# Kernel optimization log

Measured on AMD Instinct MI355X. Metric: run time of the kernel, lower is better.

The kernel has to match this reference:

```python
import jax, jax.numpy as jnp
import numpy as np

D_MODEL = 1024
N_HEADS = 16
D_K = D_MODEL // N_HEADS
B, S = 2, 2048


def setup_inputs() -> dict:
    key = jax.random.key(0)
    ks = jax.random.split(key, 5)
    sc = 1.0 / np.sqrt(D_MODEL)
    return {
        "x": jax.random.normal(ks[0], (B, S, D_MODEL), dtype=jnp.float32),
        "W_qkv": jax.random.normal(ks[1], (D_MODEL, 3 * D_MODEL), dtype=jnp.float32) * sc,
        "b_qkv": jnp.zeros((3 * D_MODEL,), dtype=jnp.float32),
        "W_out": jax.random.normal(ks[2], (D_MODEL, D_MODEL), dtype=jnp.float32) * sc,
        "b_out": jnp.zeros((D_MODEL,), dtype=jnp.float32),
    }


def reference(x, W_qkv, b_qkv, W_out, b_out):
    Bb, Ss, _ = x.shape
    qkv = x @ W_qkv + b_qkv                     # [B,S,3*D]
    qkv = qkv.reshape(Bb, Ss, 3, N_HEADS, D_K)
    qkv = jnp.transpose(qkv, (2, 0, 3, 1, 4))   # [3,B,H,S,Dk]
    q, k, v = qkv[0], qkv[1], qkv[2]
    scale = jnp.asarray(np.sqrt(D_K), dtype=x.dtype)
    attn = jnp.einsum('bhsd,bhtd->bhst', q, k) / scale  # [B,H,S,S]
    attn = jax.nn.softmax(attn, axis=-1)
    out = jnp.einsum('bhst,bhtd->bhsd', attn, v)        # [B,H,S,Dk]
    out = jnp.transpose(out, (0, 2, 1, 3)).reshape(Bb, Ss, D_MODEL)
    return out @ W_out + b_out
```

## Files before the change

### kernel.cpp

```cpp
#include <hip/hip_runtime.h>

typedef __bf16 bf16x8 __attribute__((ext_vector_type(8)));
typedef __bf16 bf16x4 __attribute__((ext_vector_type(4)));
typedef float f32x4 __attribute__((ext_vector_type(4)));
typedef unsigned short u16;
typedef unsigned short u16x4 __attribute__((ext_vector_type(4)));
typedef unsigned int u32;

__device__ __forceinline__ u16 f2bu(float f) {
  __bf16 h = (__bf16)f;
  return __builtin_bit_cast(u16, h);
}

__device__ __forceinline__ void gld16(const u16* g, const __bf16* lds) {
  __builtin_amdgcn_global_load_lds(
      (const __attribute__((address_space(1))) u32*)(uintptr_t)g,
      (__attribute__((address_space(3))) u32*)(u32)(uintptr_t)lds, 16, 0, 0);
}

__device__ __forceinline__ void tr_tile(const float* __restrict__ in, u16* __restrict__ out,
                                        int R, int C, int bx, int by, int tid) {
  __shared__ u16 t[64][65];
  int tx = tid & 63, ty = tid >> 6;
  int r0 = by * 64, c0 = bx * 64;
  for (int i = 0; i < 16; ++i)
    t[ty + i * 4][tx] = f2bu(in[(size_t)(r0 + ty + i * 4) * C + c0 + tx]);
  __syncthreads();
  for (int i = 0; i < 16; ++i)
    out[(size_t)(c0 + ty + i * 4) * R + r0 + tx] = t[tx][ty + i * 4];
}

__global__ __launch_bounds__(256) void prep(const float* __restrict__ Wqkv,
                                            u16* __restrict__ Wqkv_t,
                                            const float* __restrict__ Wout,
                                            u16* __restrict__ Wout_t,
                                            const float* __restrict__ x,
                                            u16* __restrict__ xb) {
  int id = blockIdx.x, tid = threadIdx.x;
  if (id < 768) {
    tr_tile(Wqkv, Wqkv_t, 1024, 3072, id % 48, id / 48, tid);
  } else if (id < 1024) {
    int id2 = id - 768;
    tr_tile(Wout, Wout_t, 1024, 1024, id2 % 16, id2 / 16, tid);
  } else {
    size_t i = ((size_t)(id - 1024) * 256 + tid) * 8;
    f32x4 a0 = *(const f32x4*)(x + i);
    f32x4 a1 = *(const f32x4*)(x + i + 4);
    bf16x8 v;
    for (int j = 0; j < 4; ++j) { v[j] = (__bf16)a0[j]; v[j + 4] = (__bf16)a1[j]; }
    *(bf16x8*)(xb + i) = v;
  }
}

template <int MODE, int TM, int TN, int MT, int NT, int XM, int XN>
__global__ __launch_bounds__(256) void gemm_bt(const u16* __restrict__ A,
                                               const u16* __restrict__ Bt,
                                               const float* __restrict__ bias,
                                               void* __restrict__ O0v,
                                               u16* __restrict__ O1,
                                               u16* __restrict__ O2,
                                               int M, int N, int K) {
  constexpr int NI = TM / 32;
  constexpr int NJ = TN / 32;
  constexpr int AE = TM * 32;
  constexpr int BE = TN * 32;
  __shared__ __bf16 smem[2 * (AE + BE)];

  int tid = threadIdx.x;
  int w = tid >> 6, lane = tid & 63, quad = lane >> 4, l16 = lane & 15;
  int wr = w >> 1, wc = w & 1;

  int id = blockIdx.x;
  int xcd = id & 7, s0i = id >> 3;
  int mg = xcd % (MT / XM), ng = xcd / (MT / XM);
  int sm = s0i % XM, sn = s0i / XM;
  int m0 = (mg * XM + sm) * TM, n0 = (ng * XN + sn) * TN;

  int srow = w * 16 + (lane >> 2);
  int sch = (lane & 3) ^ ((lane >> 3) & 3);
  const u16* Ag = A + (size_t)(m0 + srow) * K + sch * 8;
  const u16* Bg = Bt + (size_t)(n0 + srow) * K + sch * 8;

  int swl = (quad ^ ((l16 >> 1) & 3)) << 3;

  f32x4 acc[NI][NJ] = {};

#define GLD_STEP(c, kk)                                                          \
  {                                                                              \
    for (int p = 0; p < TM / 64; ++p)                                            \
      gld16(Ag + (size_t)p * 64 * K + (kk), smem + (c) * (AE + BE) + w * 512 + p * 2048); \
    for (int p = 0; p < TN / 64; ++p)                                            \
      gld16(Bg + (size_t)p * 64 * K + (kk), smem + (c) * (AE + BE) + AE + w * 512 + p * 2048); \
  }

  GLD_STEP(0, 0);
  int NS = K / 32;
  for (int s = 0; s < NS; ++s) {
    int cur = s & 1;
    __syncthreads();
    if (s + 1 < NS) GLD_STEP(1 - cur, (s + 1) * 32);
    const __bf16* Asub = smem + cur * (AE + BE);
    const __bf16* Bsub = Asub + AE;
    bf16x8 af[NI], bfr[NJ];
    for (int i = 0; i < NI; ++i)
      af[i] = *(const bf16x8*)(Asub + (wr * (TM / 2) + i * 16 + l16) * 32 + swl);
    for (int j = 0; j < NJ; ++j)
      bfr[j] = *(const bf16x8*)(Bsub + (wc * (TN / 2) + j * 16 + l16) * 32 + swl);
    for (int i = 0; i < NI; ++i)
      for (int j = 0; j < NJ; ++j)
        acc[i][j] = __builtin_amdgcn_mfma_f32_16x16x32_bf16(af[i], bfr[j], acc[i][j], 0, 0, 0);
  }
#undef GLD_STEP

  if (MODE == 0) {
    float* O0 = (float*)O0v;
    for (int j = 0; j < NJ; ++j) {
      int n = n0 + wc * (TN / 2) + j * 16 + l16;
      float bv = bias[n];
      for (int i = 0; i < NI; ++i) {
        int mb = m0 + wr * (TM / 2) + i * 16 + quad * 4;
        for (int r = 0; r < 4; ++r)
          O0[(size_t)(mb + r) * N + n] = acc[i][j][r] + bv;
      }
    }
  } else {
    u16* O0 = (u16*)O0v;
    constexpr float QSC = 0.125f * 1.44269504f;
    for (int j = 0; j < NJ; ++j) {
      int n = n0 + wc * (TN / 2) + j * 16 + l16;
      int which = n >> 10, rem = n & 1023, h = rem >> 6, d = rem & 63;
      float bv = bias[n];
      for (int i = 0; i < NI; ++i) {
        int m = m0 + wr * (TM / 2) + i * 16 + quad * 4;
        int b = m >> 11, s = m & 2047;
        if (which == 2) {
          u16x4 val;
          for (int r = 0; r < 4; ++r) val[r] = f2bu(acc[i][j][r] + bv);
          *(u16x4*)(O2 + (((size_t)(b * 16 + h)) * 64 + d) * 2048 + s) = val;
        } else {
          u16* Od = which ? O1 : O0;
          float sc = which ? 1.f : QSC;
          for (int r = 0; r < 4; ++r)
            Od[(((size_t)(b * 16 + h)) * 2048 + (s + r)) * 64 + d] = f2bu((acc[i][j][r] + bv) * sc);
        }
      }
    }
  }
}

__global__ __launch_bounds__(256, 2) void flash_attn(const u16* __restrict__ Q,
                                                     const u16* __restrict__ K,
                                                     const u16* __restrict__ Vt,
                                                     u16* __restrict__ AO) {
  constexpr int S = 2048;
  __shared__ __bf16 Ks[2][64 * 64];
  __shared__ __bf16 Vs[2][64 * 64];
  __shared__ __bf16 Ps[4][32 * 64];

  int bh = blockIdx.x, qbase = blockIdx.y * 128;
  int tid = threadIdx.x, w = tid >> 6, lane = tid & 63, quad = lane >> 4, l16 = lane & 15;

  const u16* Qh = Q + (size_t)bh * S * 64;
  const u16* Kh = K + (size_t)bh * S * 64;
  const u16* Vh = Vt + (size_t)bh * 64 * S;

  int qrowA = qbase + w * 32 + l16;
  int qrowB = qrowA + 16;
  bf16x8 qf0a = *(const bf16x8*)(Qh + (size_t)qrowA * 64 + quad * 8);
  bf16x8 qf1a = *(const bf16x8*)(Qh + (size_t)qrowA * 64 + 32 + quad * 8);
  bf16x8 qf0b = *(const bf16x8*)(Qh + (size_t)qrowB * 64 + quad * 8);
  bf16x8 qf1b = *(const bf16x8*)(Qh + (size_t)qrowB * 64 + 32 + quad * 8);

  bf16x8 vone;
#pragma unroll
  for (int j = 0; j < 8; ++j) vone[j] = (__bf16)1.0f;

  int r0s = tid >> 3, b0s = tid & 7;
  int r1s = r0s + 32;
  int ko0 = r0s * 64 + ((b0s ^ (r0s & 7)) << 3);
  int ko1 = r1s * 64 + ((b0s ^ (r1s & 7)) << 3);

  bf16x8 kr0, kr1, vr0, vr1;
#define LOAD_TILE(tb)                                                   \
  {                                                                     \
    kr0 = *(const bf16x8*)(Kh + (size_t)((tb) + r0s) * 64 + b0s * 8);   \
    kr1 = *(const bf16x8*)(Kh + (size_t)((tb) + r1s) * 64 + b0s * 8);   \
    vr0 = *(const bf16x8*)(Vh + (size_t)r0s * S + (tb) + b0s * 8);      \
    vr1 = *(const bf16x8*)(Vh + (size_t)r1s * S + (tb) + b0s * 8);      \
  }
#define STORE_TILE(c)                                                   \
  {                                                                     \
    *(bf16x8*)(&Ks[c][ko0]) = kr0;                                      \
    *(bf16x8*)(&Ks[c][ko1]) = kr1;                                      \
    *(bf16x8*)(&Vs[c][ko0]) = vr0;                                      \
    *(bf16x8*)(&Vs[c][ko1]) = vr1;                                      \
  }

  LOAD_TILE(0);
  STORE_TILE(0);
  LOAD_TILE(64);
  __syncthreads();

  f32x4 oA[4] = {};
  f32x4 oB[4] = {};
  f32x4 lfA = {};
  f32x4 lfB = {};
  int xr = l16 & 7;
  int pw_baseA = l16 * 64 + (quad & 1) * 4;
  int pw_baseB = (l16 + 16) * 64 + (quad & 1) * 4;
  int pw_blk = quad >> 1;

  for (int it = 0; it < S / 64; ++it) {
    int c = it & 1;
    if (it + 1 < S / 64) STORE_TILE(1 - c);
    if (it + 2 < S / 64) LOAD_TILE((it + 2) * 64);

    for (int nt = 0; nt < 4; ++nt) {
      const __bf16* kb = &Ks[c][(nt * 16 + l16) * 64];
      bf16x8 kf0 = *(const bf16x8*)(kb + ((quad ^ xr) << 3));
      bf16x8 kf1 = *(const bf16x8*)(kb + (((quad + 4) ^ xr) << 3));
      f32x4 ca = {0.f, 0.f, 0.f, 0.f};
      f32x4 cb = {0.f, 0.f, 0.f, 0.f};
      ca = __builtin_amdgcn_mfma_f32_16x16x32_bf16(kf0, qf0a, ca, 0, 0, 0);
      cb = __builtin_amdgcn_mfma_f32_16x16x32_bf16(kf0, qf0b, cb, 0, 0, 0);
      ca = __builtin_amdgcn_mfma_f32_16x16x32_bf16(kf1, qf1a, ca, 0, 0, 0);
      cb = __builtin_amdgcn_mfma_f32_16x16x32_bf16(kf1, qf1b, cb, 0, 0, 0);
      bf16x4 pka, pkb;
#pragma unroll
      for (int r = 0; r < 4; ++r) {
        pka[r] = (__bf16)__builtin_amdgcn_exp2f(ca[r]);
        pkb[r] = (__bf16)__builtin_amdgcn_exp2f(cb[r]);
      }
      int pc = (((nt * 2 + pw_blk) ^ xr) << 3);
      *(bf16x4*)(&Ps[w][pw_baseA + pc]) = pka;
      *(bf16x4*)(&Ps[w][pw_baseB + pc]) = pkb;
    }

    bf16x8 pf0a = *(const bf16x8*)(&Ps[w][l16 * 64 + ((quad ^ xr) << 3)]);
    bf16x8 pf1a = *(const bf16x8*)(&Ps[w][l16 * 64 + (((quad + 4) ^ xr) << 3)]);
    bf16x8 pf0b = *(const bf16x8*)(&Ps[w][(l16 + 16) * 64 + ((quad ^ xr) << 3)]);
    bf16x8 pf1b = *(const bf16x8*)(&Ps[w][(l16 + 16) * 64 + (((quad + 4) ^ xr) << 3)]);

    lfA = __builtin_amdgcn_mfma_f32_16x16x32_bf16(pf0a, vone, lfA, 0, 0, 0);
    lfA = __builtin_amdgcn_mfma_f32_16x16x32_bf16(pf1a, vone, lfA, 0, 0, 0);
    lfB = __builtin_amdgcn_mfma_f32_16x16x32_bf16(pf0b, vone, lfB, 0, 0, 0);
    lfB = __builtin_amdgcn_mfma_f32_16x16x32_bf16(pf1b, vone, lfB, 0, 0, 0);

    for (int dt = 0; dt < 4; ++dt) {
      const __bf16* vb = &Vs[c][(dt * 16 + l16) * 64];
      bf16x8 v0 = *(const bf16x8*)(vb + ((quad ^ xr) << 3));
      bf16x8 v1 = *(const bf16x8*)(vb + (((quad + 4) ^ xr) << 3));
      oA[dt] = __builtin_amdgcn_mfma_f32_16x16x32_bf16(pf0a, v0, oA[dt], 0, 0, 0);
      oB[dt] = __builtin_amdgcn_mfma_f32_16x16x32_bf16(pf0b, v0, oB[dt], 0, 0, 0);
      oA[dt] = __builtin_amdgcn_mfma_f32_16x16x32_bf16(pf1a, v1, oA[dt], 0, 0, 0);
      oB[dt] = __builtin_amdgcn_mfma_f32_16x16x32_bf16(pf1b, v1, oB[dt], 0, 0, 0);
    }
    __syncthreads();
  }
#undef LOAD_TILE
#undef STORE_TILE

  float linvA[4], linvB[4];
#pragma unroll
  for (int r = 0; r < 4; ++r) {
    linvA[r] = 1.f / lfA[r];
    linvB[r] = 1.f / lfB[r];
  }

  int b = bh >> 4, h = bh & 15;
  for (int dt = 0; dt < 4; ++dt)
    for (int r = 0; r < 4; ++r) {
      int sA = qbase + w * 32 + quad * 4 + r;
      int sB = sA + 16;
      int d = dt * 16 + l16;
      AO[(((size_t)b * 2048 + sA) * 16 + h) * 64 + d] = f2bu(oA[dt][r] * linvA[r]);
      AO[(((size_t)b * 2048 + sB) * 16 + h) * 64 + d] = f2bu(oB[dt][r] * linvB[r]);
    }
}

extern "C" void kernel_launch(void* const* d_in, const int* in_sizes, int n_in,
                              void* d_out, int out_size, void* d_ws, size_t ws_size,
                              hipStream_t stream) {
  const float* x    = (const float*)d_in[0];
  const float* Wqkv = (const float*)d_in[1];
  const float* bqkv = (const float*)d_in[2];
  const float* Wout = (const float*)d_in[3];
  const float* bout = (const float*)d_in[4];
  float* out = (float*)d_out;

  u16* ws = (u16*)d_ws;
  size_t off = 0;
  u16* Wqkv_t = ws + off; off += (size_t)3072 * 1024;
  u16* Wout_t = ws + off; off += (size_t)1024 * 1024;
  u16* xb     = ws + off; off += (size_t)4096 * 1024;
  u16* Qb     = ws + off; off += (size_t)32 * 2048 * 64;
  u16* Kb     = ws + off; off += (size_t)32 * 2048 * 64;
  u16* Vtb    = ws + off; off += (size_t)32 * 2048 * 64;
  u16* AO     = xb;

  prep<<<dim3(3072), 256, 0, stream>>>(Wqkv, Wqkv_t, Wout, Wout_t, x, xb);
  gemm_bt<1, 128, 128, 32, 24, 8, 12><<<dim3(768), 256, 0, stream>>>(
      xb, Wqkv_t, bqkv, (void*)Qb, Kb, Vtb, 4096, 3072, 1024);
  flash_attn<<<dim3(32, 16), 256, 0, stream>>>(Qb, Kb, Vtb, AO);
  gemm_bt<0, 128, 64, 32, 16, 8, 8><<<dim3(512), 256, 0, stream>>>(
      AO, Wout_t, bout, (void*)out, nullptr, nullptr, 4096, 1024, 1024);
}
```

Measured before the change: 178.0 us.

## Redistribute softmax probabilities with cross-lane permutes instead of LDS round-trip

```diff
diff --git a/kernel.cpp b/kernel.cpp
--- a/kernel.cpp
+++ b/kernel.cpp
@@ -2,10 +2,13 @@
 
 typedef __bf16 bf16x8 __attribute__((ext_vector_type(8)));
 typedef __bf16 bf16x4 __attribute__((ext_vector_type(4)));
+typedef __bf16 bf16x2 __attribute__((ext_vector_type(2)));
 typedef float f32x4 __attribute__((ext_vector_type(4)));
 typedef unsigned short u16;
 typedef unsigned short u16x4 __attribute__((ext_vector_type(4)));
 typedef unsigned int u32;
+typedef unsigned int u32x2 __attribute__((ext_vector_type(2)));
+typedef unsigned int u32x4 __attribute__((ext_vector_type(4)));
 
 __device__ __forceinline__ u16 f2bu(float f) {
   __bf16 h = (__bf16)f;
@@ -155,7 +158,6 @@
   constexpr int S = 2048;
   __shared__ __bf16 Ks[2][64 * 64];
   __shared__ __bf16 Vs[2][64 * 64];
-  __shared__ __bf16 Ps[4][32 * 64];
 
   int bh = blockIdx.x, qbase = blockIdx.y * 128;
   int tid = threadIdx.x, w = tid >> 6, lane = tid & 63, quad = lane >> 4, l16 = lane & 15;
@@ -206,15 +208,14 @@
   f32x4 lfA = {};
   f32x4 lfB = {};
   int xr = l16 & 7;
-  int pw_baseA = l16 * 64 + (quad & 1) * 4;
-  int pw_baseB = (l16 + 16) * 64 + (quad & 1) * 4;
-  int pw_blk = quad >> 1;
 
   for (int it = 0; it < S / 64; ++it) {
     int c = it & 1;
     if (it + 1 < S / 64) STORE_TILE(1 - c);
     if (it + 2 < S / 64) LOAD_TILE((it + 2) * 64);
 
+    u32 pwA[4][2], pwB[4][2];
+#pragma unroll
     for (int nt = 0; nt < 4; ++nt) {
       const __bf16* kb = &Ks[c][(nt * 16 + l16) * 64];
       bf16x8 kf0 = *(const bf16x8*)(kb + ((quad ^ xr) << 3));
@@ -225,35 +226,51 @@
       cb = __builtin_amdgcn_mfma_f32_16x16x32_bf16(kf0, qf0b, cb, 0, 0, 0);
       ca = __builtin_amdgcn_mfma_f32_16x16x32_bf16(kf1, qf1a, ca, 0, 0, 0);
       cb = __builtin_amdgcn_mfma_f32_16x16x32_bf16(kf1, qf1b, cb, 0, 0, 0);
-      bf16x4 pka, pkb;
-#pragma unroll
-      for (int r = 0; r < 4; ++r) {
-        pka[r] = (__bf16)__builtin_amdgcn_exp2f(ca[r]);
-        pkb[r] = (__bf16)__builtin_amdgcn_exp2f(cb[r]);
+      bf16x2 a01 = {(__bf16)__builtin_amdgcn_exp2f(ca[0]), (__bf16)__builtin_amdgcn_exp2f(ca[1])};
+      bf16x2 a23 = {(__bf16)__builtin_amdgcn_exp2f(ca[2]), (__bf16)__builtin_amdgcn_exp2f(ca[3])};
+      bf16x2 b01 = {(__bf16)__builtin_amdgcn_exp2f(cb[0]), (__bf16)__builtin_amdgcn_exp2f(cb[1])};
+      bf16x2 b23 = {(__bf16)__builtin_amdgcn_exp2f(cb[2]), (__bf16)__builtin_amdgcn_exp2f(cb[3])};
+      pwA[nt][0] = __builtin_bit_cast(u32, a01);
+      pwA[nt][1] = __builtin_bit_cast(u32, a23);
+      pwB[nt][0] = __builtin_bit_cast(u32, b01);
+      pwB[nt][1] = __builtin_bit_cast(u32, b23);
+    }
+
+    bf16x8 pfA[2], pfB[2];
+#pragma unroll
+    for (int h = 0; h < 2; ++h) {
+      u32 GA[2], HA[2], GB[2], HB[2];
+#pragma unroll
+      for (int w2 = 0; w2 < 2; ++w2) {
+        u32x2 s1a = __builtin_amdgcn_permlane32_swap(pwA[2 * h][w2], pwA[2 * h + 1][w2], false, false);
+        u32x2 s2a = __builtin_amdgcn_permlane16_swap(s1a[0], s1a[1], false, false);
+        GA[w2] = s2a[0];
+        HA[w2] = s2a[1];
+        u32x2 s1b = __builtin_amdgcn_permlane32_swap(pwB[2 * h][w2], pwB[2 * h + 1][w2], false, false);
+        u32x2 s2b = __builtin_amdgcn_permlane16_swap(s1b[0], s1b[1], false, false);
+        GB[w2] = s2b[0];
+        HB[w2] = s2b[1];
       }
-      int pc = (((nt * 2 + pw_blk) ^ xr) << 3);
-      *(bf16x4*)(&Ps[w][pw_baseA + pc]) = pka;
-      *(bf16x4*)(&Ps[w][pw_baseB + pc]) = pkb;
-    }
-
-    bf16x8 pf0a = *(const bf16x8*)(&Ps[w][l16 * 64 + ((quad ^ xr) << 3)]);
-    bf16x8 pf1a = *(const bf16x8*)(&Ps[w][l16 * 64 + (((quad + 4) ^ xr) << 3)]);
-    bf16x8 pf0b = *(const bf16x8*)(&Ps[w][(l16 + 16) * 64 + ((quad ^ xr) << 3)]);
-    bf16x8 pf1b = *(const bf16x8*)(&Ps[w][(l16 + 16) * 64 + (((quad + 4) ^ xr) << 3)]);
-
-    lfA = __builtin_amdgcn_mfma_f32_16x16x32_bf16(pf0a, vone, lfA, 0, 0, 0);
-    lfA = __builtin_amdgcn_mfma_f32_16x16x32_bf16(pf1a, vone, lfA, 0, 0, 0);
-    lfB = __builtin_amdgcn_mfma_f32_16x16x32_bf16(pf0b, vone, lfB, 0, 0, 0);
-    lfB = __builtin_amdgcn_mfma_f32_16x16x32_bf16(pf1b, vone, lfB, 0, 0, 0);
-
+      u32x4 pa = {GA[0], GA[1], HA[0], HA[1]};
+      u32x4 pb = {GB[0], GB[1], HB[0], HB[1]};
+      pfA[h] = __builtin_bit_cast(bf16x8, pa);
+      pfB[h] = __builtin_bit_cast(bf16x8, pb);
+    }
+
+    lfA = __builtin_amdgcn_mfma_f32_16x16x32_bf16(pfA[0], vone, lfA, 0, 0, 0);
+    lfA = __builtin_amdgcn_mfma_f32_16x16x32_bf16(pfA[1], vone, lfA, 0, 0, 0);
+    lfB = __builtin_amdgcn_mfma_f32_16x16x32_bf16(pfB[0], vone, lfB, 0, 0, 0);
+    lfB = __builtin_amdgcn_mfma_f32_16x16x32_bf16(pfB[1], vone, lfB, 0, 0, 0);
+
+#pragma unroll
     for (int dt = 0; dt < 4; ++dt) {
       const __bf16* vb = &Vs[c][(dt * 16 + l16) * 64];
       bf16x8 v0 = *(const bf16x8*)(vb + ((quad ^ xr) << 3));
       bf16x8 v1 = *(const bf16x8*)(vb + (((quad + 4) ^ xr) << 3));
-      oA[dt] = __builtin_amdgcn_mfma_f32_16x16x32_bf16(pf0a, v0, oA[dt], 0, 0, 0);
-      oB[dt] = __builtin_amdgcn_mfma_f32_16x16x32_bf16(pf0b, v0, oB[dt], 0, 0, 0);
-      oA[dt] = __builtin_amdgcn_mfma_f32_16x16x32_bf16(pf1a, v1, oA[dt], 0, 0, 0);
-      oB[dt] = __builtin_amdgcn_mfma_f32_16x16x32_bf16(pf1b, v1, oB[dt], 0, 0, 0);
+      oA[dt] = __builtin_amdgcn_mfma_f32_16x16x32_bf16(pfA[0], v0, oA[dt], 0, 0, 0);
+      oB[dt] = __builtin_amdgcn_mfma_f32_16x16x32_bf16(pfB[0], v0, oB[dt], 0, 0, 0);
+      oA[dt] = __builtin_amdgcn_mfma_f32_16x16x32_bf16(pfA[1], v1, oA[dt], 0, 0, 0);
+      oB[dt] = __builtin_amdgcn_mfma_f32_16x16x32_bf16(pfB[1], v1, oB[dt], 0, 0, 0);
     }
     __syncthreads();
   }
```

New measurement: 173.7 us. -2.5%, faster.
